# Kernel tuning notes

Measured on AMD Instinct MI355X. Metric: run time of the kernel, lower is better.

Reference implementation:

```python
import jax, jax.numpy as jnp
import numpy as np

N_NODES = 50000
N_EDGES = 800000
IN_CH = 512
HID = 256


def setup_inputs() -> dict:
    key = jax.random.key(0)
    ks = jax.random.split(key, 8)
    x = jax.random.normal(ks[0], (N_NODES, IN_CH), dtype=jnp.float32)
    edge_index = jax.random.randint(ks[1], (2, N_EDGES), 0, N_NODES, dtype=jnp.int64)
    # Glorot-ish init for weights
    W0 = jax.random.normal(ks[2], (IN_CH, HID), dtype=jnp.float32) / np.sqrt(IN_CH)
    W1 = jax.random.normal(ks[3], (HID, HID), dtype=jnp.float32) / np.sqrt(HID)
    W2 = jax.random.normal(ks[4], (HID, HID), dtype=jnp.float32) / np.sqrt(HID)
    Wout = jax.random.normal(ks[5], (HID, 1), dtype=jnp.float32) / np.sqrt(HID)
    return {
        "x": x, "edge_index": edge_index,
        "W0": W0, "b0": jnp.zeros((HID,), jnp.float32),
        "W1": W1, "b1": jnp.zeros((HID,), jnp.float32),
        "W2": W2, "b2": jnp.zeros((HID,), jnp.float32),
        "Wout": Wout, "bout": jnp.zeros((1,), jnp.float32),
    }


def _gcn_norm(edge_index, num_nodes):
    # Add self-loops, compute symmetric normalization D^-1/2 (A+I) D^-1/2
    loops = jnp.arange(num_nodes, dtype=edge_index.dtype)
    src = jnp.concatenate([edge_index[0], loops])
    dst = jnp.concatenate([edge_index[1], loops])
    ones = jnp.ones(src.shape[0], dtype=jnp.float32)
    deg = jax.ops.segment_sum(ones, dst, num_segments=num_nodes)
    dinv = jnp.where(deg > 0, jax.lax.rsqrt(deg), 0.0)
    norm = dinv[src] * dinv[dst]  # [E + N]
    return src, dst, norm


def _gcn_conv(x, src, dst, norm, W, b, num_nodes):
    h = x @ W                              # [N, out] dense GEMM first (PyG order)
    msg = h[src] * norm[:, None]           # gather + scale
    agg = jax.ops.segment_sum(msg, dst, num_segments=num_nodes)  # scatter-add
    return agg + b


def reference(x, edge_index, W0, b0, W1, b1, W2, b2, Wout, bout):
    n = x.shape[0]
    src, dst, norm = _gcn_norm(edge_index, n)
    h = jax.nn.relu(_gcn_conv(x, src, dst, norm, W0, b0, n))
    h = jax.nn.relu(_gcn_conv(h, src, dst, norm, W1, b1, n))
    h = jax.nn.relu(_gcn_conv(h, src, dst, norm, W2, b2, n))
    out = h @ Wout + bout                  # [N, 1] readout
    return out[:, 0]                       # squeeze(-1) -> [N]
```

## Files before the change

kernel.cpp:

```cpp
#include <hip/hip_runtime.h>

#define HID 256
#define IN_CH 512
#define NPAD 50176

#define NGRAN 12
#define BTSTEP (NGRAN * 256 * 8)

typedef __attribute__((ext_vector_type(8))) short s16x8;
typedef __attribute__((ext_vector_type(4))) float f32x4;
typedef __attribute__((ext_vector_type(4))) _Float16 f16x4;

#define GLBP(p) ((const __attribute__((address_space(1))) void*)(p))
#define LDSP(p) ((__attribute__((address_space(3))) void*)(p))


__global__ __launch_bounds__(256) void k_count(const int* __restrict__ dst,
                                               int* __restrict__ cnt, int E) {
    int e = blockIdx.x * 256 + threadIdx.x;
    if (e < E) atomicAdd(&cnt[dst[e]], 1);
}

__global__ __launch_bounds__(256) void k_scan_bsum(const int* __restrict__ cnt,
                                                   int* __restrict__ bsum, int n) {
    __shared__ int sdata[256];
    int t = threadIdx.x;
    int base = blockIdx.x * 1024 + t * 4;
    int s = 0;
#pragma unroll
    for (int j = 0; j < 4; ++j) if (base + j < n) s += cnt[base + j];
    sdata[t] = s;
    __syncthreads();
    for (int off = 128; off > 0; off >>= 1) {
        if (t < off) sdata[t] += sdata[t + off];
        __syncthreads();
    }
    if (t == 0) bsum[blockIdx.x] = sdata[0];
}

__global__ __launch_bounds__(64) void k_scan_boff(const int* __restrict__ bsum,
                                                  int* __restrict__ boff, int nb) {
    int lane = threadIdx.x;
    int own = (lane < nb) ? bsum[lane] : 0;
    int v = own;
    for (int off = 1; off < 64; off <<= 1) {
        int u = __shfl_up(v, off, 64);
        if (lane >= off) v += u;
    }
    if (lane < nb) boff[lane] = v - own;
}

__global__ __launch_bounds__(256) void k_scan_write(const int* __restrict__ cnt,
                                                    const int* __restrict__ boff,
                                                    int* __restrict__ rowptr,
                                                    float* __restrict__ dinv, int n) {
    __shared__ int sdata[256];
    int t = threadIdx.x;
    int base = blockIdx.x * 1024 + t * 4;
    int c0 = (base + 0 < n) ? cnt[base + 0] : 0;
    int c1 = (base + 1 < n) ? cnt[base + 1] : 0;
    int c2 = (base + 2 < n) ? cnt[base + 2] : 0;
    int c3 = (base + 3 < n) ? cnt[base + 3] : 0;
    int tsum = c0 + c1 + c2 + c3;
    sdata[t] = tsum;
    __syncthreads();
    for (int off = 1; off < 256; off <<= 1) {
        int v = (t >= off) ? sdata[t - off] : 0;
        __syncthreads();
        if (t >= off) sdata[t] += v;
        __syncthreads();
    }
    int excl = sdata[t] - tsum;
    int p = boff[blockIdx.x] + excl;
    if (base + 0 < n) { rowptr[base + 1] = p + c0;                dinv[base + 0] = rsqrtf((float)(c0 + 1)); }
    if (base + 1 < n) { rowptr[base + 2] = p + c0 + c1;           dinv[base + 1] = rsqrtf((float)(c1 + 1)); }
    if (base + 2 < n) { rowptr[base + 3] = p + c0 + c1 + c2;      dinv[base + 2] = rsqrtf((float)(c2 + 1)); }
    if (base + 3 < n) { rowptr[base + 4] = p + c0 + c1 + c2 + c3; dinv[base + 3] = rsqrtf((float)(c3 + 1)); }
    if (blockIdx.x == 0 && t == 0) rowptr[0] = 0;
}

__global__ __launch_bounds__(256) void k_fill(const int* __restrict__ src,
                                              const int* __restrict__ dst,
                                              const int* __restrict__ rowptr,
                                              int* __restrict__ cursor,
                                              const float* __restrict__ dinv,
                                              int2* __restrict__ erec, int E) {
    int e = blockIdx.x * 256 + threadIdx.x;
    if (e >= E) return;
    int d = dst[e];
    int s = src[e];
    int pos = rowptr[d] + atomicAdd(&cursor[d], 1);
    float w = dinv[s] * dinv[d];
    erec[pos] = make_int2(s, __float_as_int(w));
}


__device__ __forceinline__ void wsplit_one(const float* W, unsigned short* Bt, int idx) {
    int n = idx & 255;
    int k = idx >> 8;
    float w = W[(size_t)k * HID + n];
    unsigned int u = __float_as_uint(w);
    unsigned short hi = (unsigned short)(u >> 16);
    float hif = __uint_as_float(u & 0xffff0000u);
    float lo = w - hif;
    unsigned short lob = (unsigned short)(__float_as_uint(lo) >> 16);
    unsigned short* base = Bt + (size_t)(k >> 5) * BTSTEP;
    int kz = k & 31;
    int e0 = 3 * kz, e1 = e0 + 1, e2 = e0 + 2;
    base[((e0 >> 3) * 256 + n) * 8 + (e0 & 7)] = hi;
    base[((e1 >> 3) * 256 + n) * 8 + (e1 & 7)] = hi;
    base[((e2 >> 3) * 256 + n) * 8 + (e2 & 7)] = lob;
}

__global__ __launch_bounds__(256) void k_wsplit3(const float* __restrict__ W0,
                                                 const float* __restrict__ W1,
                                                 const float* __restrict__ W2,
                                                 unsigned short* __restrict__ Bt0,
                                                 unsigned short* __restrict__ Bt1,
                                                 unsigned short* __restrict__ Bt2) {
    int t = blockIdx.x * 256 + threadIdx.x;
    if (t < IN_CH * HID) wsplit_one(W0, Bt0, t);
    else if (t < IN_CH * HID + HID * HID) wsplit_one(W1, Bt1, t - IN_CH * HID);
    else wsplit_one(W2, Bt2, t - IN_CH * HID - HID * HID);
}


template<bool RELU>
__global__ __launch_bounds__(512) void k_gemm_mfma(const float* __restrict__ A,
                                                   const unsigned short* __restrict__ Bt,
                                                   _Float16* __restrict__ C16,
                                                   int M, int Korig) {
    __shared__ s16x8 AlsG[NGRAN * 128];
    __shared__ s16x8 BlsG[NGRAN * 256];

    const int m0 = blockIdx.x * 128;
    const int tid = threadIdx.x;
    const int wave = tid >> 6;
    const int lane = tid & 63;
    const int wm = wave >> 2;
    const int wn = wave & 3;

    f32x4 acc[4][4] = {};

    const int nsteps = Korig >> 5;
    const int arow = tid >> 2;
    const int at   = tid & 3;

    for (int ks = 0; ks < nsteps; ++ks) {
        {
            int gm = m0 + arow;
            float4 v0 = make_float4(0, 0, 0, 0), v1 = v0;
            if (gm < M) {
                const float* ap = A + (size_t)gm * Korig + ks * 32 + at * 8;
                v0 = *(const float4*)ap;
                v1 = *(const float4*)(ap + 4);
            }
            float av[8] = {v0.x, v0.y, v0.z, v0.w, v1.x, v1.y, v1.z, v1.w};
            unsigned short hi[8], lo[8];
#pragma unroll
            for (int j = 0; j < 8; ++j) {
                float a = av[j];
                if (RELU) a = fmaxf(a, 0.f);
                unsigned int u = __float_as_uint(a);
                hi[j] = (unsigned short)(u >> 16);
                float hif = __uint_as_float(u & 0xffff0000u);
                float l = a - hif;
                lo[j] = (unsigned short)(__float_as_uint(l) >> 16);
            }
            s16x8 w0 = {(short)hi[0], (short)lo[0], (short)hi[0], (short)hi[1],
                        (short)lo[1], (short)hi[1], (short)hi[2], (short)lo[2]};
            s16x8 w1 = {(short)hi[2], (short)hi[3], (short)lo[3], (short)hi[3],
                        (short)hi[4], (short)lo[4], (short)hi[4], (short)hi[5]};
            s16x8 w2 = {(short)lo[5], (short)hi[5], (short)hi[6], (short)lo[6],
                        (short)hi[6], (short)hi[7], (short)lo[7], (short)hi[7]};
            AlsG[(3 * at + 0) * 128 + arow] = w0;
            AlsG[(3 * at + 1) * 128 + arow] = w1;
            AlsG[(3 * at + 2) * 128 + arow] = w2;
        }
        {
            const char* src = (const char*)(Bt + (size_t)ks * BTSTEP);
            for (int g = wave; g < 48; g += 8) {
                int byteoff = (g * 64 + lane) * 16;
                __builtin_amdgcn_global_load_lds(GLBP(src + byteoff),
                                                 LDSP((char*)BlsG + byteoff), 16, 0, 0);
            }
        }
        __syncthreads();

#pragma unroll
        for (int kk = 0; kk < 3; ++kk) {
            int g = kk * 4 + (lane >> 4);
            s16x8 af[4], bf[4];
#pragma unroll
            for (int mf = 0; mf < 4; ++mf) {
                int row = wm * 64 + mf * 16 + (lane & 15);
                af[mf] = AlsG[g * 128 + row];
            }
#pragma unroll
            for (int nf = 0; nf < 4; ++nf) {
                int col = wn * 64 + nf * 16 + (lane & 15);
                bf[nf] = BlsG[g * 256 + col];
            }
#pragma unroll
            for (int mf = 0; mf < 4; ++mf)
#pragma unroll
                for (int nf = 0; nf < 4; ++nf)
                    acc[mf][nf] = __builtin_amdgcn_mfma_f32_16x16x32_bf16(af[mf], bf[nf],
                                                                          acc[mf][nf], 0, 0, 0);
        }
        __syncthreads();
    }

#pragma unroll
    for (int mf = 0; mf < 4; ++mf) {
        int row0 = m0 + wm * 64 + mf * 16 + (lane >> 4) * 4;
#pragma unroll
        for (int r = 0; r < 4; ++r) {
            int gr = row0 + r;
            if (gr < M) {
#pragma unroll
                for (int nf = 0; nf < 4; ++nf) {
                    int col = wn * 64 + nf * 16 + (lane & 15);
                    C16[(size_t)gr * HID + col] = (_Float16)acc[mf][nf][r];
                }
            }
        }
    }
}


template<bool READOUT>
__global__ __launch_bounds__(256) void k_aggregate(const _Float16* __restrict__ h,
                                                   const float* __restrict__ dinv,
                                                   const int* __restrict__ rowptr,
                                                   const int2* __restrict__ erec,
                                                   const float* __restrict__ bias,
                                                   float* __restrict__ agg,
                                                   const float* __restrict__ wout,
                                                   const float* __restrict__ bout,
                                                   float* __restrict__ out,
                                                   int n) {
    int node = blockIdx.x * 4 + (threadIdx.x >> 6);
    if (node >= n) return;
    int lane = threadIdx.x & 63;

    float dd = dinv[node];
    float4 acc;
    {
        float w = dd * dd;
        f16x4 v = *(const f16x4*)(h + (size_t)node * HID + lane * 4);
        float4 b = *(const float4*)(bias + lane * 4);
        acc = make_float4(b.x + (float)v[0] * w, b.y + (float)v[1] * w,
                          b.z + (float)v[2] * w, b.w + (float)v[3] * w);
    }

    int e = rowptr[node];
    int e_end = rowptr[node + 1];
    for (; e + 1 < e_end; e += 2) {
        int2 r0 = erec[e];
        int2 r1 = erec[e + 1];
        float w0 = __int_as_float(r0.y);
        float w1 = __int_as_float(r1.y);
        f16x4 v0 = *(const f16x4*)(h + (size_t)r0.x * HID + lane * 4);
        f16x4 v1 = *(const f16x4*)(h + (size_t)r1.x * HID + lane * 4);
        acc.x += (float)v0[0] * w0 + (float)v1[0] * w1;
        acc.y += (float)v0[1] * w0 + (float)v1[1] * w1;
        acc.z += (float)v0[2] * w0 + (float)v1[2] * w1;
        acc.w += (float)v0[3] * w0 + (float)v1[3] * w1;
    }
    if (e < e_end) {
        int2 r0 = erec[e];
        float w0 = __int_as_float(r0.y);
        f16x4 v0 = *(const f16x4*)(h + (size_t)r0.x * HID + lane * 4);
        acc.x += (float)v0[0] * w0; acc.y += (float)v0[1] * w0;
        acc.z += (float)v0[2] * w0; acc.w += (float)v0[3] * w0;
    }

    if (!READOUT) {
        *(float4*)(agg + (size_t)node * HID + lane * 4) = acc;
    } else {
        float4 w = *(const float4*)(wout + lane * 4);
        acc.x = fmaxf(acc.x, 0.f); acc.y = fmaxf(acc.y, 0.f);
        acc.z = fmaxf(acc.z, 0.f); acc.w = fmaxf(acc.w, 0.f);
        float s = acc.x * w.x + acc.y * w.y + acc.z * w.z + acc.w * w.w;
#pragma unroll
        for (int off = 32; off > 0; off >>= 1) s += __shfl_down(s, off, 64);
        if (lane == 0) out[node] = s + bout[0];
    }
}


extern "C" void kernel_launch(void* const* d_in, const int* in_sizes, int n_in,
                              void* d_out, int out_size, void* d_ws, size_t ws_size,
                              hipStream_t stream) {
    const float* x    = (const float*)d_in[0];
    const int*   ei   = (const int*)d_in[1];
    const float* W0   = (const float*)d_in[2];
    const float* b0   = (const float*)d_in[3];
    const float* W1   = (const float*)d_in[4];
    const float* b1   = (const float*)d_in[5];
    const float* W2   = (const float*)d_in[6];
    const float* b2   = (const float*)d_in[7];
    const float* Wout = (const float*)d_in[8];
    const float* bout = (const float*)d_in[9];
    float* out = (float*)d_out;

    const int n = in_sizes[0] / IN_CH;
    const int E = in_sizes[1] / 2;
    const int* src = ei;
    const int* dst = ei + E;

    float* dinv   = (float*)d_ws;
    int*   rowptr = (int*)(dinv + NPAD);
    int*   cursor = rowptr + NPAD;
    int2*  erec   = (int2*)(cursor + NPAD);
    int*   bsum   = (int*)(erec + 800000);
    int*   boff   = bsum + 64;
    unsigned short* Bt0 = (unsigned short*)(boff + 64);
    unsigned short* Bt1 = Bt0 + 16 * BTSTEP;
    unsigned short* Bt2 = Bt1 + 8 * BTSTEP;
    _Float16* h16 = (_Float16*)(Bt2 + 8 * BTSTEP);
    float* agg32  = (float*)(h16 + (size_t)n * HID);

    const int nb_e = (E + 255) / 256;
    const int nb_scan = (n + 1023) / 1024;

    hipMemsetAsync(cursor, 0, (size_t)n * 4, stream);
    k_count<<<nb_e, 256, 0, stream>>>(dst, cursor, E);
    k_scan_bsum<<<nb_scan, 256, 0, stream>>>(cursor, bsum, n);
    k_scan_boff<<<1, 64, 0, stream>>>(bsum, boff, nb_scan);
    k_scan_write<<<nb_scan, 256, 0, stream>>>(cursor, boff, rowptr, dinv, n);
    hipMemsetAsync(cursor, 0, (size_t)n * 4, stream);
    k_fill<<<nb_e, 256, 0, stream>>>(src, dst, rowptr, cursor, dinv, erec, E);

    k_wsplit3<<<(IN_CH * HID + 2 * HID * HID) / 256, 256, 0, stream>>>(W0, W1, W2, Bt0, Bt1, Bt2);

    const int gemm_blocks = (n + 127) / 128;
    const int agg_blocks = (n + 3) / 4;

    k_gemm_mfma<false><<<gemm_blocks, 512, 0, stream>>>(x, Bt0, h16, n, IN_CH);
    k_aggregate<false><<<agg_blocks, 256, 0, stream>>>(h16, dinv, rowptr, erec, b0,
                                                       agg32, nullptr, nullptr, nullptr, n);
    k_gemm_mfma<true><<<gemm_blocks, 512, 0, stream>>>(agg32, Bt1, h16, n, HID);
    k_aggregate<false><<<agg_blocks, 256, 0, stream>>>(h16, dinv, rowptr, erec, b1,
                                                       agg32, nullptr, nullptr, nullptr, n);
    k_gemm_mfma<true><<<gemm_blocks, 512, 0, stream>>>(agg32, Bt2, h16, n, HID);
    k_aggregate<true><<<agg_blocks, 256, 0, stream>>>(h16, dinv, rowptr, erec, b2,
                                                      nullptr, Wout, bout, out, n);
}
```

Before: 545.9 us.

## Replace split-bf16 GEMM with fp16 MFMA and pre-tiled fp16 aggregate output

Drops the 3-term bf16 hi/lo emulation of fp32 GEMM and uses a single fp16 MFMA pass, which cuts MFMA work and LDS traffic by about 3x. The aggregate kernel now applies ReLU and writes fp16 directly in the GEMM's tiled LDS layout, so later GEMMs can stream A with global_load_lds instead of loading fp32 and converting it. Weights are converted once to fp16 in the matching layout. The trade is lower precision in the GEMM inputs, which could exceed the accuracy tolerance.

```diff
diff --git a/kernel.cpp b/kernel.cpp
--- a/kernel.cpp
+++ b/kernel.cpp
@@ -4,12 +4,13 @@
 #define IN_CH 512
 #define NPAD 50176
 
-#define NGRAN 12
-#define BTSTEP (NGRAN * 256 * 8)
-
-typedef __attribute__((ext_vector_type(8))) short s16x8;
+#define A_STEP_SHORTS 4096
+#define B_STEP_SHORTS 8192
+#define AGGT_TILE_SHORTS 32768
+
+typedef __attribute__((ext_vector_type(8))) _Float16 f16x8;
+typedef __attribute__((ext_vector_type(4))) _Float16 f16x4;
 typedef __attribute__((ext_vector_type(4))) float f32x4;
-typedef __attribute__((ext_vector_type(4))) _Float16 f16x4;
 
 #define GLBP(p) ((const __attribute__((address_space(1))) void*)(p))
 #define LDSP(p) ((__attribute__((address_space(3))) void*)(p))
@@ -95,43 +96,35 @@
 }
 
 
-__device__ __forceinline__ void wsplit_one(const float* W, unsigned short* Bt, int idx) {
+__device__ __forceinline__ void wcvt_one(const float* W, _Float16* Wt, int idx) {
     int n = idx & 255;
     int k = idx >> 8;
-    float w = W[(size_t)k * HID + n];
-    unsigned int u = __float_as_uint(w);
-    unsigned short hi = (unsigned short)(u >> 16);
-    float hif = __uint_as_float(u & 0xffff0000u);
-    float lo = w - hif;
-    unsigned short lob = (unsigned short)(__float_as_uint(lo) >> 16);
-    unsigned short* base = Bt + (size_t)(k >> 5) * BTSTEP;
-    int kz = k & 31;
-    int e0 = 3 * kz, e1 = e0 + 1, e2 = e0 + 2;
-    base[((e0 >> 3) * 256 + n) * 8 + (e0 & 7)] = hi;
-    base[((e1 >> 3) * 256 + n) * 8 + (e1 & 7)] = hi;
-    base[((e2 >> 3) * 256 + n) * 8 + (e2 & 7)] = lob;
-}
-
-__global__ __launch_bounds__(256) void k_wsplit3(const float* __restrict__ W0,
-                                                 const float* __restrict__ W1,
-                                                 const float* __restrict__ W2,
-                                                 unsigned short* __restrict__ Bt0,
-                                                 unsigned short* __restrict__ Bt1,
-                                                 unsigned short* __restrict__ Bt2) {
+    _Float16 v = (_Float16)W[(size_t)k * HID + n];
+    int ks = k >> 5, g = (k >> 3) & 3;
+    Wt[(((size_t)ks * 4 + g) * 256 + n) * 8 + (k & 7)] = v;
+}
+
+__global__ __launch_bounds__(256) void k_wcvt3(const float* __restrict__ W0,
+                                               const float* __restrict__ W1,
+                                               const float* __restrict__ W2,
+                                               _Float16* __restrict__ Wt0,
+                                               _Float16* __restrict__ Wt1,
+                                               _Float16* __restrict__ Wt2) {
     int t = blockIdx.x * 256 + threadIdx.x;
-    if (t < IN_CH * HID) wsplit_one(W0, Bt0, t);
-    else if (t < IN_CH * HID + HID * HID) wsplit_one(W1, Bt1, t - IN_CH * HID);
-    else wsplit_one(W2, Bt2, t - IN_CH * HID - HID * HID);
-}
-
-
-template<bool RELU>
-__global__ __launch_bounds__(512) void k_gemm_mfma(const float* __restrict__ A,
-                                                   const unsigned short* __restrict__ Bt,
-                                                   _Float16* __restrict__ C16,
-                                                   int M, int Korig) {
-    __shared__ s16x8 AlsG[NGRAN * 128];
-    __shared__ s16x8 BlsG[NGRAN * 256];
+    if (t < IN_CH * HID) wcvt_one(W0, Wt0, t);
+    else if (t < IN_CH * HID + HID * HID) wcvt_one(W1, Wt1, t - IN_CH * HID);
+    else wcvt_one(W2, Wt2, t - IN_CH * HID - HID * HID);
+}
+
+
+template<bool CVT_A>
+__global__ __launch_bounds__(512) void k_gemm16(const float* __restrict__ A32,
+                                                const _Float16* __restrict__ At,
+                                                const _Float16* __restrict__ Wt,
+                                                _Float16* __restrict__ C16,
+                                                int M, int K) {
+    __shared__ f16x8 AlsG[4 * 128];
+    __shared__ f16x8 BlsG[4 * 256];
 
     const int m0 = blockIdx.x * 128;
     const int tid = threadIdx.x;
@@ -142,55 +135,45 @@
 
     f32x4 acc[4][4] = {};
 
-    const int nsteps = Korig >> 5;
-    const int arow = tid >> 2;
-    const int at   = tid & 3;
+    const int nsteps = K >> 5;
 
     for (int ks = 0; ks < nsteps; ++ks) {
-        {
-            int gm = m0 + arow;
+        if (CVT_A) {
+            int row = tid >> 2;
+            int j   = tid & 3;
+            int gm = m0 + row;
             float4 v0 = make_float4(0, 0, 0, 0), v1 = v0;
             if (gm < M) {
-                const float* ap = A + (size_t)gm * Korig + ks * 32 + at * 8;
+                const float* ap = A32 + (size_t)gm * K + ks * 32 + j * 8;
                 v0 = *(const float4*)ap;
                 v1 = *(const float4*)(ap + 4);
             }
-            float av[8] = {v0.x, v0.y, v0.z, v0.w, v1.x, v1.y, v1.z, v1.w};
-            unsigned short hi[8], lo[8];
-#pragma unroll
-            for (int j = 0; j < 8; ++j) {
-                float a = av[j];
-                if (RELU) a = fmaxf(a, 0.f);
-                unsigned int u = __float_as_uint(a);
-                hi[j] = (unsigned short)(u >> 16);
-                float hif = __uint_as_float(u & 0xffff0000u);
-                float l = a - hif;
-                lo[j] = (unsigned short)(__float_as_uint(l) >> 16);
-            }
-            s16x8 w0 = {(short)hi[0], (short)lo[0], (short)hi[0], (short)hi[1],
-                        (short)lo[1], (short)hi[1], (short)hi[2], (short)lo[2]};
-            s16x8 w1 = {(short)hi[2], (short)hi[3], (short)lo[3], (short)hi[3],
-                        (short)hi[4], (short)lo[4], (short)hi[4], (short)hi[5]};
-            s16x8 w2 = {(short)lo[5], (short)hi[5], (short)hi[6], (short)lo[6],
-                        (short)hi[6], (short)hi[7], (short)lo[7], (short)hi[7]};
-            AlsG[(3 * at + 0) * 128 + arow] = w0;
-            AlsG[(3 * at + 1) * 128 + arow] = w1;
-            AlsG[(3 * at + 2) * 128 + arow] = w2;
+            f16x8 w;
+            w[0] = (_Float16)v0.x; w[1] = (_Float16)v0.y;
+            w[2] = (_Float16)v0.z; w[3] = (_Float16)v0.w;
+            w[4] = (_Float16)v1.x; w[5] = (_Float16)v1.y;
+            w[6] = (_Float16)v1.z; w[7] = (_Float16)v1.w;
+            AlsG[j * 128 + row] = w;
+        } else {
+            const char* asrc = (const char*)(At + ((size_t)blockIdx.x * nsteps + ks) * A_STEP_SHORTS);
+            int byteoff = tid * 16;
+            __builtin_amdgcn_global_load_lds(GLBP(asrc + byteoff),
+                                             LDSP((char*)AlsG + byteoff), 16, 0, 0);
         }
         {
-            const char* src = (const char*)(Bt + (size_t)ks * BTSTEP);
-            for (int g = wave; g < 48; g += 8) {
-                int byteoff = (g * 64 + lane) * 16;
-                __builtin_amdgcn_global_load_lds(GLBP(src + byteoff),
+            const char* bsrc = (const char*)(Wt + (size_t)ks * B_STEP_SHORTS);
+#pragma unroll
+            for (int c = 0; c < 2; ++c) {
+                int byteoff = (c * 512 + tid) * 16;
+                __builtin_amdgcn_global_load_lds(GLBP(bsrc + byteoff),
                                                  LDSP((char*)BlsG + byteoff), 16, 0, 0);
             }
         }
         __syncthreads();
 
-#pragma unroll
-        for (int kk = 0; kk < 3; ++kk) {
-            int g = kk * 4 + (lane >> 4);
-            s16x8 af[4], bf[4];
+        {
+            int g = lane >> 4;
+            f16x8 af[4], bf[4];
 #pragma unroll
             for (int mf = 0; mf < 4; ++mf) {
                 int row = wm * 64 + mf * 16 + (lane & 15);
@@ -205,8 +188,8 @@
             for (int mf = 0; mf < 4; ++mf)
 #pragma unroll
                 for (int nf = 0; nf < 4; ++nf)
-                    acc[mf][nf] = __builtin_amdgcn_mfma_f32_16x16x32_bf16(af[mf], bf[nf],
-                                                                          acc[mf][nf], 0, 0, 0);
+                    acc[mf][nf] = __builtin_amdgcn_mfma_f32_16x16x32_f16(af[mf], bf[nf],
+                                                                         acc[mf][nf], 0, 0, 0);
         }
         __syncthreads();
     }
@@ -235,7 +218,7 @@
                                                    const int* __restrict__ rowptr,
                                                    const int2* __restrict__ erec,
                                                    const float* __restrict__ bias,
-                                                   float* __restrict__ agg,
+                                                   _Float16* __restrict__ aggT,
                                                    const float* __restrict__ wout,
                                                    const float* __restrict__ bout,
                                                    float* __restrict__ out,
@@ -277,14 +260,22 @@
     }
 
     if (!READOUT) {
-        *(float4*)(agg + (size_t)node * HID + lane * 4) = acc;
+        int t = node >> 7, r = node & 127;
+        int ks = lane >> 3, g = (lane >> 1) & 3, off = (lane & 1) * 4;
+        f16x4 o;
+        o[0] = (_Float16)fmaxf(acc.x, 0.f);
+        o[1] = (_Float16)fmaxf(acc.y, 0.f);
+        o[2] = (_Float16)fmaxf(acc.z, 0.f);
+        o[3] = (_Float16)fmaxf(acc.w, 0.f);
+        _Float16* dst = aggT + (size_t)t * AGGT_TILE_SHORTS + (((ks * 4 + g) * 128 + r) * 8 + off);
+        *(f16x4*)dst = o;
     } else {
         float4 w = *(const float4*)(wout + lane * 4);
         acc.x = fmaxf(acc.x, 0.f); acc.y = fmaxf(acc.y, 0.f);
         acc.z = fmaxf(acc.z, 0.f); acc.w = fmaxf(acc.w, 0.f);
         float s = acc.x * w.x + acc.y * w.y + acc.z * w.z + acc.w * w.w;
 #pragma unroll
-        for (int off = 32; off > 0; off >>= 1) s += __shfl_down(s, off, 64);
+        for (int off2 = 32; off2 > 0; off2 >>= 1) s += __shfl_down(s, off2, 64);
         if (lane == 0) out[node] = s + bout[0];
     }
 }
@@ -310,17 +301,19 @@
     const int* src = ei;
     const int* dst = ei + E;
 
+    const int mtiles = (n + 127) / 128;
+
     float* dinv   = (float*)d_ws;
     int*   rowptr = (int*)(dinv + NPAD);
     int*   cursor = rowptr + NPAD;
     int2*  erec   = (int2*)(cursor + NPAD);
     int*   bsum   = (int*)(erec + 800000);
     int*   boff   = bsum + 64;
-    unsigned short* Bt0 = (unsigned short*)(boff + 64);
-    unsigned short* Bt1 = Bt0 + 16 * BTSTEP;
-    unsigned short* Bt2 = Bt1 + 8 * BTSTEP;
-    _Float16* h16 = (_Float16*)(Bt2 + 8 * BTSTEP);
-    float* agg32  = (float*)(h16 + (size_t)n * HID);
+    _Float16* Wt0 = (_Float16*)(boff + 64);
+    _Float16* Wt1 = Wt0 + IN_CH * HID;
+    _Float16* Wt2 = Wt1 + HID * HID;
+    _Float16* h16 = Wt2 + HID * HID;
+    _Float16* aggT = h16 + (size_t)NPAD * HID;
 
     const int nb_e = (E + 255) / 256;
     const int nb_scan = (n + 1023) / 1024;
@@ -333,18 +326,17 @@
     hipMemsetAsync(cursor, 0, (size_t)n * 4, stream);
     k_fill<<<nb_e, 256, 0, stream>>>(src, dst, rowptr, cursor, dinv, erec, E);
 
-    k_wsplit3<<<(IN_CH * HID + 2 * HID * HID) / 256, 256, 0, stream>>>(W0, W1, W2, Bt0, Bt1, Bt2);
-
-    const int gemm_blocks = (n + 127) / 128;
+    k_wcvt3<<<(IN_CH * HID + 2 * HID * HID) / 256, 256, 0, stream>>>(W0, W1, W2, Wt0, Wt1, Wt2);
+
     const int agg_blocks = (n + 3) / 4;
 
-    k_gemm_mfma<false><<<gemm_blocks, 512, 0, stream>>>(x, Bt0, h16, n, IN_CH);
+    k_gemm16<true><<<mtiles, 512, 0, stream>>>(x, nullptr, Wt0, h16, n, IN_CH);
     k_aggregate<false><<<agg_blocks, 256, 0, stream>>>(h16, dinv, rowptr, erec, b0,
-                                                       agg32, nullptr, nullptr, nullptr, n);
-    k_gemm_mfma<true><<<gemm_blocks, 512, 0, stream>>>(agg32, Bt1, h16, n, HID);
+                                                       aggT, nullptr, nullptr, nullptr, n);
+    k_gemm16<false><<<mtiles, 512, 0, stream>>>(nullptr, aggT, Wt1, h16, n, HID);
     k_aggregate<false><<<agg_blocks, 256, 0, stream>>>(h16, dinv, rowptr, erec, b1,
-                                                       agg32, nullptr, nullptr, nullptr, n);
-    k_gemm_mfma<true><<<gemm_blocks, 512, 0, stream>>>(agg32, Bt2, h16, n, HID);
+                                                       aggT, nullptr, nullptr, nullptr, n);
+    k_gemm16<false><<<mtiles, 512, 0, stream>>>(nullptr, aggT, Wt2, h16, n, HID);
     k_aggregate<true><<<agg_blocks, 256, 0, stream>>>(h16, dinv, rowptr, erec, b2,
                                                       nullptr, Wout, bout, out, n);
 }
```

Result: faster. 507.0 us (-7.1%).
